# Kernel tuning notes

Measured on AMD Instinct MI355X. Metric: run time of the kernel, lower is better.

The kernel has to match this reference:

```python
import jax, jax.numpy as jnp
import numpy as np

N_ITEMS = 200000
N_USER_TABLE = 262144
N_USERS = 16384
N_HIST = 819200
TEXT_DIM = 128
GCN_DIM = 128
HIDDEN_DIM = 256
TOWER_DIM = 128
EPS = 1e-12


def setup_inputs() -> dict:
    key = jax.random.key(0)
    ks = jax.random.split(key, 14)
    s = 0.02
    return {
        "item_text_emb": jax.random.normal(ks[0], (N_ITEMS, TEXT_DIM), jnp.float32),
        "gcn_item_emb": jax.random.normal(ks[1], (N_ITEMS, GCN_DIM), jnp.float32),
        "gcn_user_emb": jax.random.normal(ks[2], (N_USER_TABLE, GCN_DIM), jnp.float32),
        "w1_item": jax.random.normal(ks[3], (TEXT_DIM + GCN_DIM, HIDDEN_DIM), jnp.float32) * s,
        "b1_item": jax.random.normal(ks[4], (HIDDEN_DIM,), jnp.float32) * s,
        "w2_item": jax.random.normal(ks[5], (HIDDEN_DIM, TOWER_DIM), jnp.float32) * s,
        "b2_item": jax.random.normal(ks[6], (TOWER_DIM,), jnp.float32) * s,
        "w1_user": jax.random.normal(ks[7], (GCN_DIM + TOWER_DIM, HIDDEN_DIM), jnp.float32) * s,
        "b1_user": jax.random.normal(ks[8], (HIDDEN_DIM,), jnp.float32) * s,
        "w2_user": jax.random.normal(ks[9], (HIDDEN_DIM, TOWER_DIM), jnp.float32) * s,
        "b2_user": jax.random.normal(ks[10], (TOWER_DIM,), jnp.float32) * s,
        "users": jax.random.randint(ks[11], (N_USERS,), 0, N_USER_TABLE, jnp.int64),
        "hist_items": jax.random.randint(ks[12], (N_HIST,), 0, N_ITEMS, jnp.int64),
        "hist_segids": jnp.sort(jax.random.randint(ks[13], (N_HIST,), 0, N_USERS, jnp.int64)),
    }


def _l2norm(x):
    # F.normalize(x, dim=1): x / max(||x||, eps)
    n = jnp.sqrt(jnp.sum(x * x, axis=1, keepdims=True))
    return x / jnp.maximum(n, EPS)


def reference(item_text_emb, gcn_item_emb, gcn_user_emb,
              w1_item, b1_item, w2_item, b2_item,
              w1_user, b1_user, w2_user, b2_user,
              users, hist_items, hist_segids):
    # encode_items: MLP over [text || gcn] then L2 normalize
    xi = jnp.concatenate([item_text_emb, gcn_item_emb], axis=1)  # [N_ITEMS, 256]
    hi = jax.nn.relu(xi @ w1_item + b1_item)
    item_emb = _l2norm(hi @ w2_item + b2_item)  # [N_ITEMS, TOWER_DIM]

    # ragged per-user history mean pooling (segment mean over sorted segment ids)
    gathered = item_emb[hist_items]  # [N_HIST, TOWER_DIM]
    sums = jax.ops.segment_sum(gathered, hist_segids, num_segments=N_USERS,
                               indices_are_sorted=True)
    counts = jax.ops.segment_sum(jnp.ones((hist_segids.shape[0],), item_emb.dtype),
                                 hist_segids, num_segments=N_USERS,
                                 indices_are_sorted=True)
    # users with empty history -> zeros(TOWER_DIM)
    hist = jnp.where(counts[:, None] > 0, sums / jnp.maximum(counts[:, None], 1.0), 0.0)

    xu = jnp.concatenate([gcn_user_emb[users], hist], axis=1)  # [N_USERS, 256]
    hu = jax.nn.relu(xu @ w1_user + b1_user)
    user_emb = _l2norm(hu @ w2_user + b2_user)  # [N_USERS, TOWER_DIM]
    return user_emb, item_emb
```

## Files before the change

kernel.cpp:

```cpp
#include <hip/hip_runtime.h>
#include <stdint.h>

#define N_ITEMS   200000
#define N_USERS   16384
#define N_HIST    819200

typedef short bfrag8 __attribute__((ext_vector_type(8)));
typedef float ffrag4 __attribute__((ext_vector_type(4)));

__device__ __forceinline__ unsigned short f2bf(float f) {
    union { float f; unsigned int u; } v; v.f = f;
    unsigned int u = v.u;
    u += 0x7fffu + ((u >> 16) & 1u);
    return (unsigned short)(u >> 16);
}

__device__ __forceinline__ ffrag4 mfma16(bfrag8 a, bfrag8 b, ffrag4 c) {
    return __builtin_amdgcn_mfma_f32_16x16x32_bf16(a, b, c, 0, 0, 0);
}

__device__ __forceinline__ bfrag8 pack8(float4 x0, float4 x1) {
    bfrag8 o;
    o[0] = (short)f2bf(x0.x); o[1] = (short)f2bf(x0.y);
    o[2] = (short)f2bf(x0.z); o[3] = (short)f2bf(x0.w);
    o[4] = (short)f2bf(x1.x); o[5] = (short)f2bf(x1.y);
    o[6] = (short)f2bf(x1.z); o[7] = (short)f2bf(x1.w);
    return o;
}

__global__ void cvt_all_kernel(const float* __restrict__ w1i, const float* __restrict__ w2i,
                               const float* __restrict__ w1u, const float* __restrict__ w2u,
                               unsigned short* __restrict__ o1i, unsigned short* __restrict__ o2i,
                               unsigned short* __restrict__ o1u, unsigned short* __restrict__ o2u) {
    int id = blockIdx.x * 256 + threadIdx.x;
    const float* w; unsigned short* o; int N; int local;
    if (id < 65536)       { w = w1i; o = o1i; N = 256; local = id; }
    else if (id < 98304)  { w = w2i; o = o2i; N = 128; local = id - 65536; }
    else if (id < 163840) { w = w1u; o = o1u; N = 256; local = id - 98304; }
    else                  { w = w2u; o = o2u; N = 128; local = id - 163840; }
    int n = local >> 8;
    int k = local & 255;
    o[local] = f2bf(w[(size_t)k * N + n]);
}

#define LOAD_A(tt)  do { \
    int rb_ = (tt) * 32; \
    _Pragma("unroll") \
    for (int mi_ = 0; mi_ < 2; ++mi_) { \
        int r_ = rb_ + mi_ * 16 + lr; \
        int ra_ = rowIdxA ? rowIdxA[r_] : r_; \
        const float* pA_ = srcA + (size_t)ra_ * 128; \
        const float* pB_ = srcB + (size_t)r_ * 128; \
        _Pragma("unroll") \
        for (int kt_ = 0; kt_ < 8; ++kt_) { \
            const float* p_ = (kt_ < 4) ? (pA_ + kt_ * 32 + lg * 8) \
                                        : (pB_ + (kt_ - 4) * 32 + lg * 8); \
            a4[mi_][kt_][0] = ((const float4*)p_)[0]; \
            a4[mi_][kt_][1] = ((const float4*)p_)[1]; \
        } \
    } } while (0)

__global__ __launch_bounds__(256, 1) void tower2_kernel(
    const float* __restrict__ srcA, const float* __restrict__ srcB,
    const int* __restrict__ rowIdxA,
    const unsigned short* __restrict__ w1t, const float* __restrict__ b1,
    const unsigned short* __restrict__ w2t, const float* __restrict__ b2,
    float* __restrict__ out, unsigned short* __restrict__ mirror,
    int nTiles)
{
    __shared__ __align__(16) char smem[131072 + 16384];
    char* sW1 = smem;
    char* sH  = smem + 131072;
    float* sPn = (float*)(smem + 131072);

    const int tid  = threadIdx.x;
    const int lane = tid & 63;
    const int wav  = tid >> 6;
    const int lr   = lane & 15;
    const int lg   = lane >> 4;

    {
        const uint4* g = (const uint4*)w1t;
#pragma unroll
        for (int i = 0; i < 32; ++i) {
            int c = tid + 256 * i;
            int n = c >> 5, k16 = c & 31;
            uint4 v = g[c];
            *(uint4*)(sW1 + n * 512 + ((k16 * 16) ^ ((n & 7) << 4))) = v;
        }
    }

    bfrag8 w2f[2][8];
#pragma unroll
    for (int j = 0; j < 2; ++j) {
        int n2 = wav * 32 + j * 16 + lr;
#pragma unroll
        for (int kt = 0; kt < 8; ++kt)
            w2f[j][kt] = *(const bfrag8*)((const char*)w2t + (size_t)n2 * 512 + kt * 64 + lg * 16);
    }
    float b1v[4];
#pragma unroll
    for (int i = 0; i < 4; ++i) b1v[i] = b1[(wav * 4 + i) * 16 + lr];
    float b2v[2];
#pragma unroll
    for (int j = 0; j < 2; ++j) b2v[j] = b2[wav * 32 + j * 16 + lr];

    __syncthreads();

    const int stride = (int)gridDim.x;
    int t = (int)blockIdx.x;
    float4 a4[2][8][2];
    if (t < nTiles) LOAD_A(t);

    for (; t < nTiles; t += stride) {
        bfrag8 af[2][8];
#pragma unroll
        for (int mi = 0; mi < 2; ++mi)
#pragma unroll
            for (int kt = 0; kt < 8; ++kt)
                af[mi][kt] = pack8(a4[mi][kt][0], a4[mi][kt][1]);
        int tn = t + stride;
        if (tn < nTiles) LOAD_A(tn);

        ffrag4 acc[2][4];
#pragma unroll
        for (int mi = 0; mi < 2; ++mi)
#pragma unroll
            for (int i = 0; i < 4; ++i) acc[mi][i] = (ffrag4){0.f, 0.f, 0.f, 0.f};
#pragma unroll
        for (int kt = 0; kt < 8; ++kt) {
#pragma unroll
            for (int i = 0; i < 4; ++i) {
                int n = (wav * 4 + i) * 16 + lr;
                bfrag8 b = *(const bfrag8*)(sW1 + n * 512 + ((kt * 64 + lg * 16) ^ ((n & 7) << 4)));
                acc[0][i] = mfma16(af[0][kt], b, acc[0][i]);
                acc[1][i] = mfma16(af[1][kt], b, acc[1][i]);
            }
        }

#pragma unroll
        for (int i = 0; i < 4; ++i) {
            int col = (wav * 4 + i) * 16 + lr;
#pragma unroll
            for (int mi = 0; mi < 2; ++mi)
#pragma unroll
                for (int r = 0; r < 4; ++r) {
                    float v = fmaxf(acc[mi][i][r] + b1v[i], 0.f);
                    int row = mi * 16 + lg * 4 + r;
                    *(unsigned short*)(sH + row * 512 + ((col * 2) ^ ((row & 7) << 4))) = f2bf(v);
                }
        }
        __syncthreads();

        ffrag4 acc2[2][2];
#pragma unroll
        for (int m = 0; m < 2; ++m)
#pragma unroll
            for (int j = 0; j < 2; ++j) acc2[m][j] = (ffrag4){0.f, 0.f, 0.f, 0.f};
#pragma unroll
        for (int kt = 0; kt < 8; ++kt) {
#pragma unroll
            for (int m = 0; m < 2; ++m) {
                int row = m * 16 + lr;
                bfrag8 ha = *(const bfrag8*)(sH + row * 512 + ((kt * 64 + lg * 16) ^ ((row & 7) << 4)));
                acc2[m][0] = mfma16(ha, w2f[0][kt], acc2[m][0]);
                acc2[m][1] = mfma16(ha, w2f[1][kt], acc2[m][1]);
            }
        }

        float y[2][2][4];
        float pn[2][4];
#pragma unroll
        for (int m = 0; m < 2; ++m)
#pragma unroll
            for (int r = 0; r < 4; ++r) pn[m][r] = 0.f;
#pragma unroll
        for (int m = 0; m < 2; ++m)
#pragma unroll
            for (int j = 0; j < 2; ++j)
#pragma unroll
                for (int r = 0; r < 4; ++r) {
                    float v = acc2[m][j][r] + b2v[j];
                    y[m][j][r] = v;
                    pn[m][r] += v * v;
                }
#pragma unroll
        for (int m = 0; m < 2; ++m)
#pragma unroll
            for (int r = 0; r < 4; ++r) {
                float s = pn[m][r];
                s += __shfl_xor(s, 1, 16);
                s += __shfl_xor(s, 2, 16);
                s += __shfl_xor(s, 4, 16);
                s += __shfl_xor(s, 8, 16);
                pn[m][r] = s;
            }
        __syncthreads();
        if (lr == 0) {
#pragma unroll
            for (int m = 0; m < 2; ++m)
#pragma unroll
                for (int r = 0; r < 4; ++r)
                    sPn[(m * 16 + lg * 4 + r) * 4 + wav] = pn[m][r];
        }
        __syncthreads();

        int rb = t * 32;
#pragma unroll
        for (int m = 0; m < 2; ++m)
#pragma unroll
            for (int r = 0; r < 4; ++r) {
                float4 q = *(float4*)(sPn + (m * 16 + lg * 4 + r) * 4);
                float s = q.x + q.y + q.z + q.w;
                float sc = 1.f / fmaxf(sqrtf(s), 1e-12f);
                int row = rb + m * 16 + lg * 4 + r;
#pragma unroll
                for (int j = 0; j < 2; ++j) {
                    int col = wav * 32 + j * 16 + lr;
                    float v = y[m][j][r] * sc;
                    out[(size_t)row * 128 + col] = v;
                    if (mirror) mirror[(size_t)row * 128 + col] = f2bf(v);
                }
            }
        __syncthreads();
    }
}

__global__ __launch_bounds__(256) void pool2_kernel(
    const unsigned short* __restrict__ mirror,
    const float* __restrict__ itemF,
    const int* __restrict__ histItems,
    const int* __restrict__ histSeg,
    float* __restrict__ hist)
{
    const int u = blockIdx.x * 4 + (threadIdx.x >> 6);
    const int lane = threadIdx.x & 63;

    int lo = 0, hi = N_HIST;
    while (lo < hi) { int m = (lo + hi) >> 1; if (histSeg[m] < u) lo = m + 1; else hi = m; }
    const int s = lo;
    hi = N_HIST;
    while (lo < hi) { int m = (lo + hi) >> 1; if (histSeg[m] < u + 1) lo = m + 1; else hi = m; }
    const int e = lo;

    float ax = 0.f, ay = 0.f;
    if (mirror) {
        for (int i = s; i < e; ++i) {
            int idx = histItems[i];
            unsigned v = *(const unsigned*)(mirror + (size_t)idx * 128 + lane * 2);
            union { unsigned u; float f; } c0, c1;
            c0.u = v << 16; c1.u = v & 0xffff0000u;
            ax += c0.f; ay += c1.f;
        }
    } else {
        for (int i = s; i < e; ++i) {
            int idx = histItems[i];
            float2 v = *(const float2*)(itemF + (size_t)idx * 128 + lane * 2);
            ax += v.x; ay += v.y;
        }
    }
    float inv = (e > s) ? 1.f / (float)(e - s) : 0.f;
    float2 r; r.x = ax * inv; r.y = ay * inv;
    *(float2*)(hist + (size_t)u * 128 + lane * 2) = r;
}

extern "C" void kernel_launch(void* const* d_in, const int* in_sizes, int n_in,
                              void* d_out, int out_size, void* d_ws, size_t ws_size,
                              hipStream_t stream) {
    const float* text    = (const float*)d_in[0];
    const float* gcnItem = (const float*)d_in[1];
    const float* gcnUser = (const float*)d_in[2];
    const float* w1i = (const float*)d_in[3];
    const float* b1i = (const float*)d_in[4];
    const float* w2i = (const float*)d_in[5];
    const float* b2i = (const float*)d_in[6];
    const float* w1u = (const float*)d_in[7];
    const float* b1u = (const float*)d_in[8];
    const float* w2u = (const float*)d_in[9];
    const float* b2u = (const float*)d_in[10];
    const int* users     = (const int*)d_in[11];
    const int* histItems = (const int*)d_in[12];
    const int* histSeg   = (const int*)d_in[13];

    float* outUser = (float*)d_out;
    float* outItem = (float*)d_out + (size_t)N_USERS * 128;

    char* ws = (char*)d_ws;
    unsigned short* w1ti = (unsigned short*)(ws + 0);
    unsigned short* w2ti = (unsigned short*)(ws + 131072);
    unsigned short* w1tu = (unsigned short*)(ws + 196608);
    unsigned short* w2tu = (unsigned short*)(ws + 327680);
    float*          hist = (float*)(ws + 393216);
    const size_t mirrorOff = 8781824;
    const size_t needBytes = mirrorOff + (size_t)N_ITEMS * 128 * 2;
    unsigned short* mirror = (ws_size >= needBytes) ? (unsigned short*)(ws + mirrorOff) : nullptr;

    cvt_all_kernel<<<768, 256, 0, stream>>>(w1i, w2i, w1u, w2u, w1ti, w2ti, w1tu, w2tu);

    tower2_kernel<<<512, 256, 0, stream>>>(
        text, gcnItem, nullptr, w1ti, b1i, w2ti, b2i, outItem, mirror, N_ITEMS / 32);

    pool2_kernel<<<N_USERS / 4, 256, 0, stream>>>(mirror, outItem, histItems, histSeg, hist);

    tower2_kernel<<<512, 256, 0, stream>>>(
        gcnUser, hist, users, w1tu, b1u, w2tu, b2u, outUser, nullptr, N_USERS / 32);
}
```

Measured before the change: 347.2 us.

## Make each wave own a full 16-row tile and chain both GEMMs in registers

The MLP tower kernel now gives each wave an independent 16-row tile and computes all 256 hidden columns itself, with transposed MFMAs (weights as A, activations as B). The layer-1 accumulators are repacked directly into layer-2 B fragments, which removes the shared-memory hidden buffer and every per-tile __syncthreads. W2 is pre-permuted into a matching layout and read from global or L2 rather than held in registers, and the L2 norm reduces with two shuffles inside the wave. The pooling kernel splits each wave into two halves that handle alternate history items with wider loads. The trade-off is much higher register pressure (16+8 accumulators per wave) and per-tile global reads of W2.

Result: slower. 1.150 ms (+231.3%).

```diff
diff --git a/kernel.cpp b/kernel.cpp
--- a/kernel.cpp
+++ b/kernel.cpp
@@ -33,200 +33,155 @@
                                unsigned short* __restrict__ o1i, unsigned short* __restrict__ o2i,
                                unsigned short* __restrict__ o1u, unsigned short* __restrict__ o2u) {
     int id = blockIdx.x * 256 + threadIdx.x;
-    const float* w; unsigned short* o; int N; int local;
-    if (id < 65536)       { w = w1i; o = o1i; N = 256; local = id; }
-    else if (id < 98304)  { w = w2i; o = o2i; N = 128; local = id - 65536; }
-    else if (id < 163840) { w = w1u; o = o1u; N = 256; local = id - 98304; }
-    else                  { w = w2u; o = o2u; N = 128; local = id - 163840; }
-    int n = local >> 8;
-    int k = local & 255;
-    o[local] = f2bf(w[(size_t)k * N + n]);
-}
-
-#define LOAD_A(tt)  do { \
-    int rb_ = (tt) * 32; \
+    const float* w; unsigned short* o; int local; int isW2;
+    if (id < 65536)       { w = w1i; o = o1i; isW2 = 0; local = id; }
+    else if (id < 98304)  { w = w2i; o = o2i; isW2 = 1; local = id - 65536; }
+    else if (id < 163840) { w = w1u; o = o1u; isW2 = 0; local = id - 98304; }
+    else                  { w = w2u; o = o2u; isW2 = 1; local = id - 163840; }
+    if (!isW2) {
+        int n = local >> 8;
+        int k = local & 255;
+        o[local] = f2bf(w[(size_t)k * 256 + n]);
+    } else {
+        int oo  = local >> 8;
+        int rem = local & 255;
+        int kt = rem >> 5, g = (rem >> 3) & 3, j = rem & 7;
+        int k = (2 * kt + (j >> 2)) * 16 + 4 * g + (j & 3);
+        o[local] = f2bf(w[(size_t)k * 128 + oo]);
+    }
+}
+
+#define LOAD_X(tt)  do { \
+    int r_ = (tt) * 16 + lr; \
+    int ra_ = rowIdxA ? rowIdxA[r_] : r_; \
+    const float* pA_ = srcA + (size_t)ra_ * 128; \
+    const float* pB_ = srcB + (size_t)r_ * 128; \
     _Pragma("unroll") \
-    for (int mi_ = 0; mi_ < 2; ++mi_) { \
-        int r_ = rb_ + mi_ * 16 + lr; \
-        int ra_ = rowIdxA ? rowIdxA[r_] : r_; \
-        const float* pA_ = srcA + (size_t)ra_ * 128; \
-        const float* pB_ = srcB + (size_t)r_ * 128; \
-        _Pragma("unroll") \
-        for (int kt_ = 0; kt_ < 8; ++kt_) { \
-            const float* p_ = (kt_ < 4) ? (pA_ + kt_ * 32 + lg * 8) \
-                                        : (pB_ + (kt_ - 4) * 32 + lg * 8); \
-            a4[mi_][kt_][0] = ((const float4*)p_)[0]; \
-            a4[mi_][kt_][1] = ((const float4*)p_)[1]; \
-        } \
+    for (int kt_ = 0; kt_ < 8; ++kt_) { \
+        const float* p_ = (kt_ < 4) ? (pA_ + kt_ * 32 + lg * 8) \
+                                    : (pB_ + (kt_ - 4) * 32 + lg * 8); \
+        a4[kt_][0] = ((const float4*)p_)[0]; \
+        a4[kt_][1] = ((const float4*)p_)[1]; \
     } } while (0)
 
-__global__ __launch_bounds__(256, 1) void tower2_kernel(
+__global__ __launch_bounds__(512, 2) void tower3_kernel(
     const float* __restrict__ srcA, const float* __restrict__ srcB,
     const int* __restrict__ rowIdxA,
     const unsigned short* __restrict__ w1t, const float* __restrict__ b1,
-    const unsigned short* __restrict__ w2t, const float* __restrict__ b2,
+    const unsigned short* __restrict__ w2s, const float* __restrict__ b2,
     float* __restrict__ out, unsigned short* __restrict__ mirror,
     int nTiles)
 {
-    __shared__ __align__(16) char smem[131072 + 16384];
+    __shared__ __align__(16) char smem[131072 + 1024];
     char* sW1 = smem;
-    char* sH  = smem + 131072;
-    float* sPn = (float*)(smem + 131072);
+    float* sB1 = (float*)(smem + 131072);
 
     const int tid  = threadIdx.x;
     const int lane = tid & 63;
-    const int wav  = tid >> 6;
+    const int wv   = tid >> 6;
     const int lr   = lane & 15;
     const int lg   = lane >> 4;
+    const int swz  = (lr & 7) << 4;
 
     {
         const uint4* g = (const uint4*)w1t;
 #pragma unroll
-        for (int i = 0; i < 32; ++i) {
-            int c = tid + 256 * i;
+        for (int i = 0; i < 16; ++i) {
+            int c = tid + 512 * i;
             int n = c >> 5, k16 = c & 31;
-            uint4 v = g[c];
-            *(uint4*)(sW1 + n * 512 + ((k16 * 16) ^ ((n & 7) << 4))) = v;
-        }
-    }
-
-    bfrag8 w2f[2][8];
-#pragma unroll
-    for (int j = 0; j < 2; ++j) {
-        int n2 = wav * 32 + j * 16 + lr;
-#pragma unroll
-        for (int kt = 0; kt < 8; ++kt)
-            w2f[j][kt] = *(const bfrag8*)((const char*)w2t + (size_t)n2 * 512 + kt * 64 + lg * 16);
-    }
-    float b1v[4];
-#pragma unroll
-    for (int i = 0; i < 4; ++i) b1v[i] = b1[(wav * 4 + i) * 16 + lr];
-    float b2v[2];
-#pragma unroll
-    for (int j = 0; j < 2; ++j) b2v[j] = b2[wav * 32 + j * 16 + lr];
+            *(uint4*)(sW1 + n * 512 + ((k16 * 16) ^ ((n & 7) << 4))) = g[c];
+        }
+        if (tid < 256) sB1[tid] = b1[tid];
+    }
+    ffrag4 b2v[8];
+#pragma unroll
+    for (int ot = 0; ot < 8; ++ot)
+        b2v[ot] = *(const ffrag4*)(b2 + ot * 16 + 4 * lg);
 
     __syncthreads();
 
-    const int stride = (int)gridDim.x;
-    int t = (int)blockIdx.x;
-    float4 a4[2][8][2];
-    if (t < nTiles) LOAD_A(t);
+    const int stride = (int)gridDim.x * 8;
+    int t = (int)blockIdx.x * 8 + wv;
+    float4 a4[8][2];
+    if (t < nTiles) LOAD_X(t);
 
     for (; t < nTiles; t += stride) {
-        bfrag8 af[2][8];
-#pragma unroll
-        for (int mi = 0; mi < 2; ++mi)
-#pragma unroll
-            for (int kt = 0; kt < 8; ++kt)
-                af[mi][kt] = pack8(a4[mi][kt][0], a4[mi][kt][1]);
+        bfrag8 af[8];
+#pragma unroll
+        for (int kt = 0; kt < 8; ++kt) af[kt] = pack8(a4[kt][0], a4[kt][1]);
         int tn = t + stride;
-        if (tn < nTiles) LOAD_A(tn);
-
-        ffrag4 acc[2][4];
-#pragma unroll
-        for (int mi = 0; mi < 2; ++mi)
-#pragma unroll
-            for (int i = 0; i < 4; ++i) acc[mi][i] = (ffrag4){0.f, 0.f, 0.f, 0.f};
+        if (tn < nTiles) LOAD_X(tn);
+
+        ffrag4 acc1[16];
+#pragma unroll
+        for (int nt = 0; nt < 16; ++nt)
+            acc1[nt] = *(const ffrag4*)(sB1 + nt * 16 + lg * 4);
 #pragma unroll
         for (int kt = 0; kt < 8; ++kt) {
 #pragma unroll
-            for (int i = 0; i < 4; ++i) {
-                int n = (wav * 4 + i) * 16 + lr;
-                bfrag8 b = *(const bfrag8*)(sW1 + n * 512 + ((kt * 64 + lg * 16) ^ ((n & 7) << 4)));
-                acc[0][i] = mfma16(af[0][kt], b, acc[0][i]);
-                acc[1][i] = mfma16(af[1][kt], b, acc[1][i]);
-            }
-        }
-
-#pragma unroll
-        for (int i = 0; i < 4; ++i) {
-            int col = (wav * 4 + i) * 16 + lr;
-#pragma unroll
-            for (int mi = 0; mi < 2; ++mi)
-#pragma unroll
-                for (int r = 0; r < 4; ++r) {
-                    float v = fmaxf(acc[mi][i][r] + b1v[i], 0.f);
-                    int row = mi * 16 + lg * 4 + r;
-                    *(unsigned short*)(sH + row * 512 + ((col * 2) ^ ((row & 7) << 4))) = f2bf(v);
-                }
-        }
-        __syncthreads();
-
-        ffrag4 acc2[2][2];
-#pragma unroll
-        for (int m = 0; m < 2; ++m)
-#pragma unroll
-            for (int j = 0; j < 2; ++j) acc2[m][j] = (ffrag4){0.f, 0.f, 0.f, 0.f};
+            for (int nt = 0; nt < 16; ++nt) {
+                bfrag8 w1f = *(const bfrag8*)(sW1 + (nt * 16 + lr) * 512
+                                              + ((kt * 64 + lg * 16) ^ swz));
+                acc1[nt] = mfma16(w1f, af[kt], acc1[nt]);
+            }
+        }
+
+        ffrag4 acc2[8];
+#pragma unroll
+        for (int ot = 0; ot < 8; ++ot) acc2[ot] = (ffrag4){0.f, 0.f, 0.f, 0.f};
 #pragma unroll
         for (int kt = 0; kt < 8; ++kt) {
-#pragma unroll
-            for (int m = 0; m < 2; ++m) {
-                int row = m * 16 + lr;
-                bfrag8 ha = *(const bfrag8*)(sH + row * 512 + ((kt * 64 + lg * 16) ^ ((row & 7) << 4)));
-                acc2[m][0] = mfma16(ha, w2f[0][kt], acc2[m][0]);
-                acc2[m][1] = mfma16(ha, w2f[1][kt], acc2[m][1]);
-            }
-        }
-
-        float y[2][2][4];
-        float pn[2][4];
-#pragma unroll
-        for (int m = 0; m < 2; ++m)
-#pragma unroll
-            for (int r = 0; r < 4; ++r) pn[m][r] = 0.f;
-#pragma unroll
-        for (int m = 0; m < 2; ++m)
-#pragma unroll
-            for (int j = 0; j < 2; ++j)
-#pragma unroll
-                for (int r = 0; r < 4; ++r) {
-                    float v = acc2[m][j][r] + b2v[j];
-                    y[m][j][r] = v;
-                    pn[m][r] += v * v;
-                }
-#pragma unroll
-        for (int m = 0; m < 2; ++m)
+            ffrag4 lo = acc1[2 * kt], hi = acc1[2 * kt + 1];
+            bfrag8 pa;
+            pa[0] = (short)f2bf(fmaxf(lo[0], 0.f));
+            pa[1] = (short)f2bf(fmaxf(lo[1], 0.f));
+            pa[2] = (short)f2bf(fmaxf(lo[2], 0.f));
+            pa[3] = (short)f2bf(fmaxf(lo[3], 0.f));
+            pa[4] = (short)f2bf(fmaxf(hi[0], 0.f));
+            pa[5] = (short)f2bf(fmaxf(hi[1], 0.f));
+            pa[6] = (short)f2bf(fmaxf(hi[2], 0.f));
+            pa[7] = (short)f2bf(fmaxf(hi[3], 0.f));
+#pragma unroll
+            for (int ot = 0; ot < 8; ++ot) {
+                bfrag8 w2f = *(const bfrag8*)((const char*)w2s
+                                              + (size_t)(ot * 16 + lr) * 512 + kt * 64 + lg * 16);
+                acc2[ot] = mfma16(w2f, pa, acc2[ot]);
+            }
+        }
+
+        float psum = 0.f;
+#pragma unroll
+        for (int ot = 0; ot < 8; ++ot) {
 #pragma unroll
             for (int r = 0; r < 4; ++r) {
-                float s = pn[m][r];
-                s += __shfl_xor(s, 1, 16);
-                s += __shfl_xor(s, 2, 16);
-                s += __shfl_xor(s, 4, 16);
-                s += __shfl_xor(s, 8, 16);
-                pn[m][r] = s;
-            }
-        __syncthreads();
-        if (lr == 0) {
-#pragma unroll
-            for (int m = 0; m < 2; ++m)
-#pragma unroll
-                for (int r = 0; r < 4; ++r)
-                    sPn[(m * 16 + lg * 4 + r) * 4 + wav] = pn[m][r];
-        }
-        __syncthreads();
-
-        int rb = t * 32;
-#pragma unroll
-        for (int m = 0; m < 2; ++m)
-#pragma unroll
-            for (int r = 0; r < 4; ++r) {
-                float4 q = *(float4*)(sPn + (m * 16 + lg * 4 + r) * 4);
-                float s = q.x + q.y + q.z + q.w;
-                float sc = 1.f / fmaxf(sqrtf(s), 1e-12f);
-                int row = rb + m * 16 + lg * 4 + r;
-#pragma unroll
-                for (int j = 0; j < 2; ++j) {
-                    int col = wav * 32 + j * 16 + lr;
-                    float v = y[m][j][r] * sc;
-                    out[(size_t)row * 128 + col] = v;
-                    if (mirror) mirror[(size_t)row * 128 + col] = f2bf(v);
-                }
-            }
-        __syncthreads();
-    }
-}
-
-__global__ __launch_bounds__(256) void pool2_kernel(
+                float v = acc2[ot][r] + b2v[ot][r];
+                acc2[ot][r] = v;
+                psum += v * v;
+            }
+        }
+        psum += __shfl_xor(psum, 16);
+        psum += __shfl_xor(psum, 32);
+        float sc = 1.f / fmaxf(sqrtf(psum), 1e-12f);
+
+        int m = t * 16 + lr;
+        float* orow = out + (size_t)m * 128;
+#pragma unroll
+        for (int ot = 0; ot < 8; ++ot) {
+            float4 v4;
+            v4.x = acc2[ot][0] * sc; v4.y = acc2[ot][1] * sc;
+            v4.z = acc2[ot][2] * sc; v4.w = acc2[ot][3] * sc;
+            *(float4*)(orow + ot * 16 + 4 * lg) = v4;
+            if (mirror) {
+                uint2 mm;
+                mm.x = (unsigned)f2bf(v4.x) | ((unsigned)f2bf(v4.y) << 16);
+                mm.y = (unsigned)f2bf(v4.z) | ((unsigned)f2bf(v4.w) << 16);
+                *(uint2*)(mirror + (size_t)m * 128 + ot * 16 + 4 * lg) = mm;
+            }
+        }
+    }
+}
+
+__global__ __launch_bounds__(256) void pool3_kernel(
     const unsigned short* __restrict__ mirror,
     const float* __restrict__ itemF,
     const int* __restrict__ histItems,
@@ -235,6 +190,8 @@
 {
     const int u = blockIdx.x * 4 + (threadIdx.x >> 6);
     const int lane = threadIdx.x & 63;
+    const int half = lane >> 5;
+    const int c = lane & 31;
 
     int lo = 0, hi = N_HIST;
     while (lo < hi) { int m = (lo + hi) >> 1; if (histSeg[m] < u) lo = m + 1; else hi = m; }
@@ -243,25 +200,32 @@
     while (lo < hi) { int m = (lo + hi) >> 1; if (histSeg[m] < u + 1) lo = m + 1; else hi = m; }
     const int e = lo;
 
-    float ax = 0.f, ay = 0.f;
+    float s0 = 0.f, s1 = 0.f, s2 = 0.f, s3 = 0.f;
     if (mirror) {
-        for (int i = s; i < e; ++i) {
+        for (int i = s + half; i < e; i += 2) {
             int idx = histItems[i];
-            unsigned v = *(const unsigned*)(mirror + (size_t)idx * 128 + lane * 2);
-            union { unsigned u; float f; } c0, c1;
-            c0.u = v << 16; c1.u = v & 0xffff0000u;
-            ax += c0.f; ay += c1.f;
+            uint2 v = *(const uint2*)(mirror + (size_t)idx * 128 + c * 4);
+            union { unsigned u; float f; } a, b, cc, d;
+            a.u  = v.x << 16; b.u  = v.x & 0xffff0000u;
+            cc.u = v.y << 16; d.u  = v.y & 0xffff0000u;
+            s0 += a.f; s1 += b.f; s2 += cc.f; s3 += d.f;
         }
     } else {
-        for (int i = s; i < e; ++i) {
+        for (int i = s + half; i < e; i += 2) {
             int idx = histItems[i];
-            float2 v = *(const float2*)(itemF + (size_t)idx * 128 + lane * 2);
-            ax += v.x; ay += v.y;
-        }
-    }
-    float inv = (e > s) ? 1.f / (float)(e - s) : 0.f;
-    float2 r; r.x = ax * inv; r.y = ay * inv;
-    *(float2*)(hist + (size_t)u * 128 + lane * 2) = r;
+            float4 v = *(const float4*)(itemF + (size_t)idx * 128 + c * 4);
+            s0 += v.x; s1 += v.y; s2 += v.z; s3 += v.w;
+        }
+    }
+    s0 += __shfl_xor(s0, 32);
+    s1 += __shfl_xor(s1, 32);
+    s2 += __shfl_xor(s2, 32);
+    s3 += __shfl_xor(s3, 32);
+    if (half == 0) {
+        float inv = (e > s) ? 1.f / (float)(e - s) : 0.f;
+        float4 r; r.x = s0 * inv; r.y = s1 * inv; r.z = s2 * inv; r.w = s3 * inv;
+        *(float4*)(hist + (size_t)u * 128 + c * 4) = r;
+    }
 }
 
 extern "C" void kernel_launch(void* const* d_in, const int* in_sizes, int n_in,
@@ -287,21 +251,21 @@
 
     char* ws = (char*)d_ws;
     unsigned short* w1ti = (unsigned short*)(ws + 0);
-    unsigned short* w2ti = (unsigned short*)(ws + 131072);
+    unsigned short* w2si = (unsigned short*)(ws + 131072);
     unsigned short* w1tu = (unsigned short*)(ws + 196608);
-    unsigned short* w2tu = (unsigned short*)(ws + 327680);
+    unsigned short* w2su = (unsigned short*)(ws + 327680);
     float*          hist = (float*)(ws + 393216);
     const size_t mirrorOff = 8781824;
     const size_t needBytes = mirrorOff + (size_t)N_ITEMS * 128 * 2;
     unsigned short* mirror = (ws_size >= needBytes) ? (unsigned short*)(ws + mirrorOff) : nullptr;
 
-    cvt_all_kernel<<<768, 256, 0, stream>>>(w1i, w2i, w1u, w2u, w1ti, w2ti, w1tu, w2tu);
-
-    tower2_kernel<<<512, 256, 0, stream>>>(
-        text, gcnItem, nullptr, w1ti, b1i, w2ti, b2i, outItem, mirror, N_ITEMS / 32);
-
-    pool2_kernel<<<N_USERS / 4, 256, 0, stream>>>(mirror, outItem, histItems, histSeg, hist);
-
-    tower2_kernel<<<512, 256, 0, stream>>>(
-        gcnUser, hist, users, w1tu, b1u, w2tu, b2u, outUser, nullptr, N_USERS / 32);
-}
+    cvt_all_kernel<<<768, 256, 0, stream>>>(w1i, w2i, w1u, w2u, w1ti, w2si, w1tu, w2su);
+
+    tower3_kernel<<<256, 512, 0, stream>>>(
+        text, gcnItem, nullptr, w1ti, b1i, w2si, b2i, outItem, mirror, N_ITEMS / 16);
+
+    pool3_kernel<<<N_USERS / 4, 256, 0, stream>>>(mirror, outItem, histItems, histSeg, hist);
+
+    tower3_kernel<<<128, 512, 0, stream>>>(
+        gcnUser, hist, users, w1tu, b1u, w2su, b2u, outUser, nullptr, N_USERS / 16);
+}
```
